# Kernel optimization log

Hardware: AMD Instinct MI355X
Metric: run time of the kernel (lower is better)

Reference implementation:

```python
import jax, jax.numpy as jnp
import numpy as np

NUM_HEADS = 8
NUM_POINTS = 4


def _bilinear(img, xs, ys):
    """Bilinear sample with zero padding (grid_sample align_corners=False).
    img: [N, H, W, C]; xs, ys: [N, P] pixel-space coords. Returns [N, P, C]."""
    H, W = img.shape[1], img.shape[2]
    x0 = jnp.floor(xs)
    y0 = jnp.floor(ys)
    wx = xs - x0
    wy = ys - y0
    x0i = x0.astype(jnp.int32)
    y0i = y0.astype(jnp.int32)

    def g(ix, iy):
        valid = ((ix >= 0) & (ix < W) & (iy >= 0) & (iy < H)).astype(img.dtype)
        ixc = jnp.clip(ix, 0, W - 1)
        iyc = jnp.clip(iy, 0, H - 1)
        v = jax.vmap(lambda im, yy, xx: im[yy, xx])(img, iyc, ixc)  # [N,P,C]
        return v * valid[..., None]

    return (g(x0i, y0i) * ((1 - wx) * (1 - wy))[..., None]
            + g(x0i + 1, y0i) * (wx * (1 - wy))[..., None]
            + g(x0i, y0i + 1) * ((1 - wx) * wy)[..., None]
            + g(x0i + 1, y0i + 1) * (wx * wy)[..., None])


def setup_inputs() -> dict:
    key = jax.random.key(0)
    ks = jax.random.split(key, 10)
    BN, C, H, W = 12, 256, 40, 100
    nq = H * W
    hp = NUM_HEADS * NUM_POINTS
    s = 1.0 / np.sqrt(C).astype(np.float32)
    return {
        "img_feats": jax.random.normal(ks[0], (BN, C, H, W), jnp.float32),
        "warp_grid": jax.random.uniform(ks[1], (BN, H, W, 2), jnp.float32),
        "reference_points": jax.random.uniform(ks[2], (BN, nq, 1, 2), jnp.float32),
        "Wv": jax.random.normal(ks[3], (C, C), jnp.float32) * s,
        "bv": jnp.zeros((C,), jnp.float32),
        "Woff": jax.random.normal(ks[4], (C, hp * 2), jnp.float32) * 0.01,
        "boff": jax.random.normal(ks[5], (hp * 2,), jnp.float32) * 0.5,
        "Wattn": jax.random.normal(ks[6], (C, hp), jnp.float32) * 0.01,
        "battn": jnp.zeros((hp,), jnp.float32),
        "Wout": jax.random.normal(ks[7], (C, C), jnp.float32) * s,
        "bout": jnp.zeros((C,), jnp.float32),
    }


def reference(img_feats, warp_grid, reference_points,
              Wv, bv, Woff, boff, Wattn, battn, Wout, bout):
    BN, C, H, W = img_feats.shape
    heads, pts = NUM_HEADS, NUM_POINTS
    hd = C // heads
    nq = H * W

    feat = img_feats.transpose(0, 2, 3, 1)  # [BN, H, W, C]

    # BEVWarp: bilinear warp of image features at the projected grid ([0,1] normed)
    gx = warp_grid[..., 0].reshape(BN, -1) * W - 0.5
    gy = warp_grid[..., 1].reshape(BN, -1) * H - 0.5
    warped = _bilinear(feat, gx, gy)          # [BN, nq, C] -> value
    query = feat.reshape(BN, nq, C)           # flattened img feats -> query

    # MultiScaleDeformableAttention, num_levels=1
    v = (warped @ Wv + bv).reshape(BN, nq, heads, hd)
    off = (query @ Woff + boff).reshape(BN, nq, heads, pts, 2)
    attn = jax.nn.softmax((query @ Wattn + battn).reshape(BN, nq, heads, pts), axis=-1)

    norm = jnp.array([W, H], dtype=img_feats.dtype)
    loc = reference_points.reshape(BN, nq, 1, 1, 2) + off / norm  # [BN,nq,h,p,2]

    vh = v.transpose(0, 2, 1, 3).reshape(BN * heads, H, W, hd)
    lx = (loc[..., 0] * W - 0.5).transpose(0, 2, 1, 3).reshape(BN * heads, nq * pts)
    ly = (loc[..., 1] * H - 0.5).transpose(0, 2, 1, 3).reshape(BN * heads, nq * pts)
    sampled = _bilinear(vh, lx, ly).reshape(BN, heads, nq, pts, hd)

    agg = jnp.einsum('bhqpd,bqhp->bqhd', sampled, attn).reshape(BN, nq, C)
    out = agg @ Wout + bout + query  # output_proj + residual (dropout=0 at eval)
    return out.transpose(0, 2, 1).reshape(BN, C, H, W)
```

## Files before the change

kernel.cpp:

```cpp
#include <hip/hip_runtime.h>

#define DEVINL __device__ __forceinline__

typedef __attribute__((ext_vector_type(4))) float f32x4;
typedef __attribute__((ext_vector_type(8))) short short8;

constexpr int kBN = 12, kC = 256, kH = 40, kW = 100;
constexpr int kNQ = kH * kW;
constexpr int kM = kBN * kNQ;

DEVINL float bflo(uint p) { union { uint i; float f; } v; v.i = p << 16; return v.f; }
DEVINL float bfhi(uint p) { union { uint i; float f; } v; v.i = p & 0xffff0000u; return v.f; }
DEVINL ushort f2bf(float f) {
  union { float f; uint i; } v; v.f = f;
  uint i = v.i;
  return (ushort)((i + 0x7fffu + ((i >> 16) & 1u)) >> 16);
}
DEVINL uint pack2(float a, float b) { return (uint)f2bf(a) | ((uint)f2bf(b) << 16); }

DEVINL void mfma_bf16(f32x4& acc, short8 a, short8 b) {
  acc = __builtin_amdgcn_mfma_f32_16x16x32_bf16(a, b, acc, 0, 0, 0);
}

DEVINL void gload16(const ushort* g, char* lds) {
  __builtin_amdgcn_global_load_lds(
      (const __attribute__((address_space(1))) uint*)g,
      (__attribute__((address_space(3))) uint*)lds, 16, 0, 0);
}

DEVINL void acc8(float* acc, uint4 d, float wv) {
  acc[0] += wv * bflo(d.x); acc[1] += wv * bfhi(d.x);
  acc[2] += wv * bflo(d.y); acc[3] += wv * bfhi(d.y);
  acc[4] += wv * bflo(d.z); acc[5] += wv * bfhi(d.z);
  acc[6] += wv * bflo(d.w); acc[7] += wv * bfhi(d.w);
}

__global__ __launch_bounds__(256) void k_wt_all(const float* __restrict__ Wv,
                                                const float* __restrict__ Woff,
                                                const float* __restrict__ Wattn,
                                                const float* __restrict__ Wout,
                                                ushort* __restrict__ WvT,
                                                ushort* __restrict__ WoffT,
                                                ushort* __restrict__ WattnT,
                                                ushort* __restrict__ WoutT) {
  int idx = blockIdx.x * 256 + threadIdx.x;
  const float* W; ushort* WT; int N, base;
  if (idx < 65536)       { W = Wv;    WT = WvT;    N = 256; base = 0; }
  else if (idx < 81920)  { W = Woff;  WT = WoffT;  N = 64;  base = 65536; }
  else if (idx < 90112)  { W = Wattn; WT = WattnT; N = 32;  base = 81920; }
  else if (idx < 155648) { W = Wout;  WT = WoutT;  N = 256; base = 90112; }
  else return;
  int i = idx - base;
  int n = i >> 8, k = i & 255;
  WT[i] = f2bf(W[k * N + n]);
}

__global__ __launch_bounds__(256) void k_transpose(const float* __restrict__ img,
                                                   ushort* __restrict__ feat) {
  __shared__ ushort tile[64][66];
  int b = blockIdx.z, c0 = blockIdx.y * 64, q0 = blockIdx.x * 64;
  int t = threadIdx.x;
  int ql = t & 63, cl = t >> 6;
#pragma unroll
  for (int i = 0; i < 16; ++i) {
    int c = cl + i * 4, q = q0 + ql;
    float v = (q < kNQ) ? img[(size_t)(b * kC + c0 + c) * kNQ + q] : 0.f;
    tile[c][ql] = f2bf(v);
  }
  __syncthreads();
#pragma unroll
  for (int i = 0; i < 2; ++i) {
    int idx = t + i * 256;
    int qlo = idx >> 3, cg = idx & 7;
    int q = q0 + qlo;
    if (q < kNQ) {
      ushort tmp[8];
#pragma unroll
      for (int j = 0; j < 8; ++j) tmp[j] = tile[cg * 8 + j][qlo];
      *(uint4*)(feat + ((size_t)b * kNQ + q) * kC + c0 + cg * 8) = *(uint4*)tmp;
    }
  }
}

__global__ __launch_bounds__(256) void k_warp(const ushort* __restrict__ feat,
                                              const float* __restrict__ grid,
                                              ushort* __restrict__ warped) {
  int orig = blockIdx.x;
  int n = (orig & 7) * 750 + (orig >> 3);
  int t = threadIdx.x;
  int ql = t >> 5, g = t & 31;
  int gq = n * 8 + ql;
  int b = gq / kNQ;
  float gx = grid[(size_t)gq * 2 + 0] * kW - 0.5f;
  float gy = grid[(size_t)gq * 2 + 1] * kH - 0.5f;
  float x0f = floorf(gx), y0f = floorf(gy);
  int x0 = (int)x0f, y0 = (int)y0f;
  float wx = gx - x0f, wy = gy - y0f;
  float acc[8];
#pragma unroll
  for (int i = 0; i < 8; ++i) acc[i] = 0.f;
  const ushort* fb = feat + (size_t)b * kNQ * kC + g * 8;
#pragma unroll
  for (int ty = 0; ty < 2; ++ty) {
    int iy = y0 + ty;
    if (iy < 0 || iy >= kH) continue;
    float wyv = ty ? wy : 1.f - wy;
#pragma unroll
    for (int tx = 0; tx < 2; ++tx) {
      int ix = x0 + tx;
      if (ix < 0 || ix >= kW) continue;
      float wv = wyv * (tx ? wx : 1.f - wx);
      uint4 d = *(const uint4*)(fb + (size_t)(iy * kW + ix) * kC);
      acc8(acc, d, wv);
    }
  }
  uint o[4] = {pack2(acc[0], acc[1]), pack2(acc[2], acc[3]),
               pack2(acc[4], acc[5]), pack2(acc[6], acc[7])};
  *(uint4*)(warped + (size_t)gq * kC + g * 8) = *(uint4*)o;
}

template <int EPI>
__global__ __launch_bounds__(256) void k_gemm256(const ushort* __restrict__ A,
                                                 const ushort* __restrict__ BT,
                                                 const float* __restrict__ bias,
                                                 ushort* __restrict__ Obf,
                                                 float* __restrict__ Ofp,
                                                 const float* __restrict__ resid) {
  extern __shared__ char smem[];
  const int t = threadIdx.x, wave = t >> 6, lane = t & 63;
  const int l15 = lane & 15, l4 = lane >> 4;
  const int b = blockIdx.x / 63, mb = blockIdx.x % 63;
  const int q0 = mb * 64;
  const int nrows = (kNQ - q0 < 64) ? (kNQ - q0) : 64;
  const int n0w = wave * 64;
  const int ra = t >> 2, ca = t & 3;
  const int rac = (ra < nrows) ? ra : (nrows - 1);
  const int sca = ca ^ ((ra >> 1) & 3);
  const ushort* gA = A + ((size_t)b * kNQ + q0 + rac) * 256 + sca * 8;
  const ushort* gB = BT + (size_t)ra * 256 + sca * 8;

  f32x4 acc[4][4];
#pragma unroll
  for (int i = 0; i < 4; ++i)
#pragma unroll
    for (int j = 0; j < 4; ++j) acc[i][j] = (f32x4)0.f;

  auto STAGE = [&](int buf, int kk) {
    char* Asb = smem + buf * 20480;
    char* Bsb = Asb + 4096;
    gload16(gA + kk, Asb + t * 16);
#pragma unroll
    for (int i = 0; i < 4; ++i)
      gload16(gB + (size_t)i * 64 * 256 + kk, Bsb + (i * 256 + t) * 16);
  };

  STAGE(0, 0);
  int cur = 0;
#pragma unroll 1
  for (int step = 0; step < 8; ++step) {
    if (step < 7) {
      STAGE(cur ^ 1, (step + 1) * 32);
      asm volatile("s_waitcnt vmcnt(5)" ::: "memory");
    } else {
      asm volatile("s_waitcnt vmcnt(0)" ::: "memory");
    }
    __builtin_amdgcn_s_barrier();
    asm volatile("" ::: "memory");
    char* Asb = smem + cur * 20480;
    char* Bsb = Asb + 4096;
    short8 af[4], bf[4];
#pragma unroll
    for (int mf = 0; mf < 4; ++mf) {
      int r = mf * 16 + l15;
      int sl = l4 ^ ((r >> 1) & 3);
      af[mf] = *(const short8*)(Asb + r * 64 + sl * 16);
    }
#pragma unroll
    for (int nf = 0; nf < 4; ++nf) {
      int r = n0w + nf * 16 + l15;
      int sl = l4 ^ ((r >> 1) & 3);
      bf[nf] = *(const short8*)(Bsb + r * 64 + sl * 16);
    }
#pragma unroll
    for (int mf = 0; mf < 4; ++mf)
#pragma unroll
      for (int nf = 0; nf < 4; ++nf) mfma_bf16(acc[mf][nf], af[mf], bf[nf]);
    asm volatile("" ::: "memory");
    __builtin_amdgcn_s_barrier();
    cur ^= 1;
  }

  if (EPI == 0) {
#pragma unroll
    for (int mf = 0; mf < 4; ++mf) {
      if (mf * 16 >= nrows) continue;
      int q = q0 + mf * 16 + l4 * 4;
#pragma unroll
      for (int nf = 0; nf < 4; ++nf) {
        int col = n0w + nf * 16 + l15;
        float bv = bias[col];
        int h = col >> 5, ch = col & 31;
        ushort* dst = Obf + (size_t)(b * 8 + h) * kNQ * 32 + ch;
#pragma unroll
        for (int j = 0; j < 4; ++j)
          dst[(size_t)(q + j) * 32] = f2bf(acc[mf][nf][j] + bv);
      }
    }
  } else {
    float* Tw = (float*)(smem + wave * 4352);
#pragma unroll
    for (int nf = 0; nf < 4; ++nf) {
      float bv = bias[n0w + nf * 16 + l15];
#pragma unroll
      for (int mf = 0; mf < 4; ++mf)
#pragma unroll
        for (int j = 0; j < 4; ++j)
          Tw[l15 * 68 + mf * 16 + l4 * 4 + j] = acc[mf][nf][j] + bv;
      int c = l15, rs = l4 * 16;
      if (rs < nrows) {
        int col = n0w + nf * 16 + c;
        size_t gi = ((size_t)b * kC + col) * kNQ + q0 + rs;
#pragma unroll
        for (int k = 0; k < 4; ++k) {
          float4 tv = *(float4*)(&Tw[c * 68 + rs + k * 4]);
          float4 rv = *(const float4*)(resid + gi + k * 4);
          tv.x += rv.x; tv.y += rv.y; tv.z += rv.z; tv.w += rv.w;
          *(float4*)(Ofp + gi + k * 4) = tv;
        }
      }
    }
  }
}

__global__ __launch_bounds__(256) void k_offattn(const ushort* __restrict__ A,
                                                 const ushort* __restrict__ WoffT,
                                                 const ushort* __restrict__ WattnT,
                                                 const float* __restrict__ boff,
                                                 const float* __restrict__ battn,
                                                 const float* __restrict__ refp,
                                                 float* __restrict__ samp) {
  extern __shared__ char smem[];
  float* T = (float*)smem;
  const int t = threadIdx.x, wave = t >> 6, lane = t & 63;
  const int l15 = lane & 15, l4 = lane >> 4;
  const int b = blockIdx.x / 63, mb = blockIdx.x % 63;
  const int q0 = mb * 64;
  const int nrows = (kNQ - q0 < 64) ? (kNQ - q0) : 64;
  const int wr = wave >> 1, wc = wave & 1;
  const int ra = t >> 2, ca = t & 3;
  const int rac = (ra < nrows) ? ra : (nrows - 1);
  const int sca = ca ^ ((ra >> 1) & 3);
  const ushort* gA  = A + ((size_t)b * kNQ + q0 + rac) * 256 + sca * 8;
  const ushort* gB0 = WoffT + (size_t)ra * 256 + sca * 8;
  const ushort* gB1 = WattnT + (size_t)ra * 256 + sca * 8;

  f32x4 acc[2][3];
#pragma unroll
  for (int i = 0; i < 2; ++i)
#pragma unroll
    for (int j = 0; j < 3; ++j) acc[i][j] = (f32x4)0.f;

  auto STAGE = [&](int buf, int kk) {
    char* Asb = smem + buf * 10240;
    char* Bsb = Asb + 4096;
    gload16(gA + kk, Asb + t * 16);
    gload16(gB0 + kk, Bsb + t * 16);
    if (t < 128) gload16(gB1 + kk, Bsb + (256 + t) * 16);
  };

  STAGE(0, 0);
  int cur = 0;
#pragma unroll 1
  for (int step = 0; step < 8; ++step) {
    if (step < 7) {
      STAGE(cur ^ 1, (step + 1) * 32);
      if (wave < 2) asm volatile("s_waitcnt vmcnt(3)" ::: "memory");
      else          asm volatile("s_waitcnt vmcnt(2)" ::: "memory");
    } else {
      asm volatile("s_waitcnt vmcnt(0)" ::: "memory");
    }
    __builtin_amdgcn_s_barrier();
    asm volatile("" ::: "memory");
    char* Asb = smem + cur * 10240;
    char* Bsb = Asb + 4096;
    short8 af[2], bf[3];
#pragma unroll
    for (int mf = 0; mf < 2; ++mf) {
      int r = wr * 32 + mf * 16 + l15;
      int sl = l4 ^ ((r >> 1) & 3);
      af[mf] = *(const short8*)(Asb + r * 64 + sl * 16);
    }
#pragma unroll
    for (int nf = 0; nf < 3; ++nf) {
      int r = wc * 48 + nf * 16 + l15;
      int sl = l4 ^ ((r >> 1) & 3);
      bf[nf] = *(const short8*)(Bsb + r * 64 + sl * 16);
    }
#pragma unroll
    for (int mf = 0; mf < 2; ++mf)
#pragma unroll
      for (int nf = 0; nf < 3; ++nf) mfma_bf16(acc[mf][nf], af[mf], bf[nf]);
    asm volatile("" ::: "memory");
    __builtin_amdgcn_s_barrier();
    cur ^= 1;
  }

#pragma unroll
  for (int nf = 0; nf < 3; ++nf) {
    int col = wc * 48 + nf * 16 + l15;
    float bv = (col < 64) ? boff[col] : battn[col - 64];
#pragma unroll
    for (int mf = 0; mf < 2; ++mf)
#pragma unroll
      for (int j = 0; j < 4; ++j) {
        int row = wr * 32 + mf * 16 + l4 * 4 + j;
        T[row * 101 + col] = acc[mf][nf][j] + bv;
      }
  }
  __syncthreads();
  int row = t >> 2;
  if (row < nrows) {
    int q = q0 + row;
    float refx = refp[((size_t)b * kNQ + q) * 2 + 0] * kW - 0.5f;
    float refy = refp[((size_t)b * kNQ + q) * 2 + 1] * kH - 0.5f;
#pragma unroll
    for (int hi2 = 0; hi2 < 2; ++hi2) {
      int h = (t & 3) + hi2 * 4;
      float sx[4], sy[4], lg[4];
#pragma unroll
      for (int p = 0; p < 4; ++p) {
        sx[p] = refx + T[row * 101 + h * 8 + p * 2 + 0];
        sy[p] = refy + T[row * 101 + h * 8 + p * 2 + 1];
        lg[p] = T[row * 101 + 64 + h * 4 + p];
      }
      float mx = fmaxf(fmaxf(lg[0], lg[1]), fmaxf(lg[2], lg[3]));
      float e[4], s = 0.f;
#pragma unroll
      for (int p = 0; p < 4; ++p) { e[p] = __expf(lg[p] - mx); s += e[p]; }
      float inv = 1.f / s;
      float* dst = samp + (((size_t)(b * 8 + h) * kNQ + q) * 4) * 3;
#pragma unroll
      for (int p = 0; p < 4; ++p) {
        dst[p * 3 + 0] = sx[p];
        dst[p * 3 + 1] = sy[p];
        dst[p * 3 + 2] = e[p] * inv;
      }
    }
  }
}

__global__ __launch_bounds__(256) void k_sample(const ushort* __restrict__ v,
                                                const float* __restrict__ samp,
                                                ushort* __restrict__ agg) {
  int orig = blockIdx.x;
  int n = (orig & 7) * 756 + (orig >> 3);
  int plane = n / 63, chunk = n - plane * 63;
  int t = threadIdx.x;
  int ql = t >> 2, g = t & 3;
  int q = chunk * 64 + ql;
  if (q >= kNQ) return;
  int b = plane >> 3, h = plane & 7;
  const ushort* pv = v + (size_t)plane * kNQ * 32 + g * 8;
  const int lane = t & 63, gbase = lane & ~3;

  const float* sp = samp + (((size_t)plane * kNQ + q) * 4 + g) * 3;
  float myx = sp[0], myy = sp[1], myw = sp[2];
  float acc[8];
#pragma unroll
  for (int i = 0; i < 8; ++i) acc[i] = 0.f;
#pragma unroll
  for (int p = 0; p < 4; ++p) {
    float sxp = __shfl(myx, gbase + p);
    float syp = __shfl(myy, gbase + p);
    float wp  = __shfl(myw, gbase + p);
    float x0f = floorf(sxp), y0f = floorf(syp);
    int x0 = (int)x0f, y0 = (int)y0f;
    float wx = sxp - x0f, wy = syp - y0f;
#pragma unroll
    for (int ty = 0; ty < 2; ++ty) {
      int iy = y0 + ty;
      if (iy < 0 || iy >= kH) continue;
      float wyv = ty ? wy : 1.f - wy;
#pragma unroll
      for (int tx = 0; tx < 2; ++tx) {
        int ix = x0 + tx;
        if (ix < 0 || ix >= kW) continue;
        float wv = wp * wyv * (tx ? wx : 1.f - wx);
        uint4 d = *(const uint4*)(pv + (size_t)(iy * kW + ix) * 32);
        acc8(acc, d, wv);
      }
    }
  }
  uint o[4] = {pack2(acc[0], acc[1]), pack2(acc[2], acc[3]),
               pack2(acc[4], acc[5]), pack2(acc[6], acc[7])};
  *(uint4*)(agg + ((size_t)b * kNQ + q) * kC + h * 32 + g * 8) = *(uint4*)o;
}

extern "C" void kernel_launch(void* const* d_in, const int* in_sizes, int n_in,
                              void* d_out, int out_size, void* d_ws, size_t ws_size,
                              hipStream_t stream) {
  const float* img   = (const float*)d_in[0];
  const float* grid  = (const float*)d_in[1];
  const float* refp  = (const float*)d_in[2];
  const float* Wv    = (const float*)d_in[3];
  const float* bv    = (const float*)d_in[4];
  const float* Woff  = (const float*)d_in[5];
  const float* boff  = (const float*)d_in[6];
  const float* Wattn = (const float*)d_in[7];
  const float* battn = (const float*)d_in[8];
  const float* Wout  = (const float*)d_in[9];
  const float* bout  = (const float*)d_in[10];
  float* out = (float*)d_out;

  char* ws = (char*)d_ws;
  const size_t SZ = (size_t)kM * kC * 2;
  ushort* feat   = (ushort*)(ws);
  ushort* warped = (ushort*)(ws + SZ);
  ushort* vbuf   = (ushort*)(ws + 2 * SZ);
  float*  samp   = (float*)(ws + 3 * SZ);
  ushort* WvT    = (ushort*)(ws + 4 * SZ);
  ushort* WoffT  = (ushort*)(ws + 4 * SZ + 131072);
  ushort* WattnT = (ushort*)(ws + 4 * SZ + 131072 + 32768);
  ushort* WoutT  = (ushort*)(ws + 4 * SZ + 131072 + 32768 + 16384);
  ushort* aggb   = warped;

  k_wt_all<<<608, 256, 0, stream>>>(Wv, Woff, Wattn, Wout, WvT, WoffT, WattnT, WoutT);
  k_transpose<<<dim3(63, 4, 12), 256, 0, stream>>>(img, feat);
  k_warp<<<6000, 256, 0, stream>>>(feat, grid, warped);
  k_gemm256<0><<<756, 256, 40960, stream>>>(warped, WvT, bv, vbuf, nullptr, nullptr);
  k_offattn<<<756, 256, 25856, stream>>>(feat, WoffT, WattnT, boff, battn, refp, samp);
  k_sample<<<6048, 256, 0, stream>>>(vbuf, samp, aggb);
  k_gemm256<1><<<756, 256, 40960, stream>>>(aggb, WoutT, bout, nullptr, out, img);
}
```

Baseline: 122.6 us.

## Merge prep, warp and offset/attention kernels; read residual from bf16 features

Combines the input transpose with weight conversion into one launch, and the bilinear warp with the offset/attention GEMM into one launch via block-index dispatch. This cuts the launch count and lets independent stages overlap. The output GEMM now reads the residual from the bf16 transposed feature buffer instead of fp32 input. That lowers precision and uses strided 2-byte loads. Warp blocks now also reserve shared memory they do not use, which may reduce occupancy.

Result: faster. 115.0 us (-6.2%).

```diff
diff --git a/kernel.cpp b/kernel.cpp
--- a/kernel.cpp
+++ b/kernel.cpp
@@ -35,97 +35,216 @@
   acc[6] += wv * bflo(d.w); acc[7] += wv * bfhi(d.w);
 }
 
-__global__ __launch_bounds__(256) void k_wt_all(const float* __restrict__ Wv,
-                                                const float* __restrict__ Woff,
-                                                const float* __restrict__ Wattn,
-                                                const float* __restrict__ Wout,
-                                                ushort* __restrict__ WvT,
-                                                ushort* __restrict__ WoffT,
-                                                ushort* __restrict__ WattnT,
-                                                ushort* __restrict__ WoutT) {
-  int idx = blockIdx.x * 256 + threadIdx.x;
-  const float* W; ushort* WT; int N, base;
-  if (idx < 65536)       { W = Wv;    WT = WvT;    N = 256; base = 0; }
-  else if (idx < 81920)  { W = Woff;  WT = WoffT;  N = 64;  base = 65536; }
-  else if (idx < 90112)  { W = Wattn; WT = WattnT; N = 32;  base = 81920; }
-  else if (idx < 155648) { W = Wout;  WT = WoutT;  N = 256; base = 90112; }
-  else return;
-  int i = idx - base;
-  int n = i >> 8, k = i & 255;
-  WT[i] = f2bf(W[k * N + n]);
-}
-
-__global__ __launch_bounds__(256) void k_transpose(const float* __restrict__ img,
-                                                   ushort* __restrict__ feat) {
+__global__ __launch_bounds__(256) void k_prep(const float* __restrict__ img,
+                                              ushort* __restrict__ feat,
+                                              const float* __restrict__ Wv,
+                                              const float* __restrict__ Woff,
+                                              const float* __restrict__ Wattn,
+                                              const float* __restrict__ Wout,
+                                              ushort* __restrict__ WvT,
+                                              ushort* __restrict__ WoffT,
+                                              ushort* __restrict__ WattnT,
+                                              ushort* __restrict__ WoutT) {
   __shared__ ushort tile[64][66];
-  int b = blockIdx.z, c0 = blockIdx.y * 64, q0 = blockIdx.x * 64;
-  int t = threadIdx.x;
-  int ql = t & 63, cl = t >> 6;
-#pragma unroll
-  for (int i = 0; i < 16; ++i) {
-    int c = cl + i * 4, q = q0 + ql;
-    float v = (q < kNQ) ? img[(size_t)(b * kC + c0 + c) * kNQ + q] : 0.f;
-    tile[c][ql] = f2bf(v);
+  int bx = blockIdx.x, t = threadIdx.x;
+  if (bx < 3024) {
+    int qb = bx % 63, cb = (bx / 63) & 3, b = bx / 252;
+    int c0 = cb * 64, q0 = qb * 64;
+    int ql = t & 63, cl = t >> 6;
+#pragma unroll
+    for (int i = 0; i < 16; ++i) {
+      int c = cl + i * 4, q = q0 + ql;
+      float v = (q < kNQ) ? img[(size_t)(b * kC + c0 + c) * kNQ + q] : 0.f;
+      tile[c][ql] = f2bf(v);
+    }
+    __syncthreads();
+#pragma unroll
+    for (int i = 0; i < 2; ++i) {
+      int idx = t + i * 256;
+      int qlo = idx >> 3, cg = idx & 7;
+      int q = q0 + qlo;
+      if (q < kNQ) {
+        ushort tmp[8];
+#pragma unroll
+        for (int j = 0; j < 8; ++j) tmp[j] = tile[cg * 8 + j][qlo];
+        *(uint4*)(feat + ((size_t)b * kNQ + q) * kC + c0 + cg * 8) = *(uint4*)tmp;
+      }
+    }
+  } else {
+    int idx = (bx - 3024) * 256 + t;
+    const float* W; ushort* WT; int N, base;
+    if (idx < 65536)       { W = Wv;    WT = WvT;    N = 256; base = 0; }
+    else if (idx < 81920)  { W = Woff;  WT = WoffT;  N = 64;  base = 65536; }
+    else if (idx < 90112)  { W = Wattn; WT = WattnT; N = 32;  base = 81920; }
+    else if (idx < 155648) { W = Wout;  WT = WoutT;  N = 256; base = 90112; }
+    else return;
+    int i = idx - base;
+    int n = i >> 8, k = i & 255;
+    WT[i] = f2bf(W[k * N + n]);
+  }
+}
+
+__global__ __launch_bounds__(256) void k_warp_offattn(const ushort* __restrict__ feat,
+                                                      const float* __restrict__ grid,
+                                                      ushort* __restrict__ warped,
+                                                      const ushort* __restrict__ WoffT,
+                                                      const ushort* __restrict__ WattnT,
+                                                      const float* __restrict__ boff,
+                                                      const float* __restrict__ battn,
+                                                      const float* __restrict__ refp,
+                                                      float* __restrict__ samp) {
+  extern __shared__ char smem[];
+  const int t = threadIdx.x;
+  int bx = blockIdx.x;
+
+  if (bx >= 756) {
+    int orig = bx - 756;
+    int n = (orig & 7) * 750 + (orig >> 3);
+    int ql = t >> 5, g = t & 31;
+    int gq = n * 8 + ql;
+    int b = gq / kNQ;
+    float gx = grid[(size_t)gq * 2 + 0] * kW - 0.5f;
+    float gy = grid[(size_t)gq * 2 + 1] * kH - 0.5f;
+    float x0f = floorf(gx), y0f = floorf(gy);
+    int x0 = (int)x0f, y0 = (int)y0f;
+    float wx = gx - x0f, wy = gy - y0f;
+    float acc[8];
+#pragma unroll
+    for (int i = 0; i < 8; ++i) acc[i] = 0.f;
+    const ushort* fb = feat + (size_t)b * kNQ * kC + g * 8;
+#pragma unroll
+    for (int ty = 0; ty < 2; ++ty) {
+      int iy = y0 + ty;
+      if (iy < 0 || iy >= kH) continue;
+      float wyv = ty ? wy : 1.f - wy;
+#pragma unroll
+      for (int tx = 0; tx < 2; ++tx) {
+        int ix = x0 + tx;
+        if (ix < 0 || ix >= kW) continue;
+        float wv = wyv * (tx ? wx : 1.f - wx);
+        uint4 d = *(const uint4*)(fb + (size_t)(iy * kW + ix) * kC);
+        acc8(acc, d, wv);
+      }
+    }
+    uint o[4] = {pack2(acc[0], acc[1]), pack2(acc[2], acc[3]),
+                 pack2(acc[4], acc[5]), pack2(acc[6], acc[7])};
+    *(uint4*)(warped + (size_t)gq * kC + g * 8) = *(uint4*)o;
+    return;
+  }
+
+  float* T = (float*)smem;
+  const int wave = t >> 6, lane = t & 63;
+  const int l15 = lane & 15, l4 = lane >> 4;
+  const int b = bx / 63, mb = bx % 63;
+  const int q0 = mb * 64;
+  const int nrows = (kNQ - q0 < 64) ? (kNQ - q0) : 64;
+  const int wr = wave >> 1, wc = wave & 1;
+  const int ra = t >> 2, ca = t & 3;
+  const int rac = (ra < nrows) ? ra : (nrows - 1);
+  const int sca = ca ^ ((ra >> 1) & 3);
+  const ushort* gA  = feat + ((size_t)b * kNQ + q0 + rac) * 256 + sca * 8;
+  const ushort* gB0 = WoffT + (size_t)ra * 256 + sca * 8;
+  const ushort* gB1 = WattnT + (size_t)ra * 256 + sca * 8;
+
+  f32x4 acc[2][3];
+#pragma unroll
+  for (int i = 0; i < 2; ++i)
+#pragma unroll
+    for (int j = 0; j < 3; ++j) acc[i][j] = (f32x4)0.f;
+
+  auto STAGE = [&](int buf, int kk) {
+    char* Asb = smem + buf * 10240;
+    char* Bsb = Asb + 4096;
+    gload16(gA + kk, Asb + t * 16);
+    gload16(gB0 + kk, Bsb + t * 16);
+    if (t < 128) gload16(gB1 + kk, Bsb + (256 + t) * 16);
+  };
+
+  STAGE(0, 0);
+  int cur = 0;
+#pragma unroll 1
+  for (int step = 0; step < 8; ++step) {
+    if (step < 7) {
+      STAGE(cur ^ 1, (step + 1) * 32);
+      if (wave < 2) asm volatile("s_waitcnt vmcnt(3)" ::: "memory");
+      else          asm volatile("s_waitcnt vmcnt(2)" ::: "memory");
+    } else {
+      asm volatile("s_waitcnt vmcnt(0)" ::: "memory");
+    }
+    __builtin_amdgcn_s_barrier();
+    asm volatile("" ::: "memory");
+    char* Asb = smem + cur * 10240;
+    char* Bsb = Asb + 4096;
+    short8 af[2], bf[3];
+#pragma unroll
+    for (int mf = 0; mf < 2; ++mf) {
+      int r = wr * 32 + mf * 16 + l15;
+      int sl = l4 ^ ((r >> 1) & 3);
+      af[mf] = *(const short8*)(Asb + r * 64 + sl * 16);
+    }
+#pragma unroll
+    for (int nf = 0; nf < 3; ++nf) {
+      int r = wc * 48 + nf * 16 + l15;
+      int sl = l4 ^ ((r >> 1) & 3);
+      bf[nf] = *(const short8*)(Bsb + r * 64 + sl * 16);
+    }
+#pragma unroll
+    for (int mf = 0; mf < 2; ++mf)
+#pragma unroll
+      for (int nf = 0; nf < 3; ++nf) mfma_bf16(acc[mf][nf], af[mf], bf[nf]);
+    asm volatile("" ::: "memory");
+    __builtin_amdgcn_s_barrier();
+    cur ^= 1;
+  }
+
+#pragma unroll
+  for (int nf = 0; nf < 3; ++nf) {
+    int col = wc * 48 + nf * 16 + l15;
+    float bv = (col < 64) ? boff[col] : battn[col - 64];
+#pragma unroll
+    for (int mf = 0; mf < 2; ++mf)
+#pragma unroll
+      for (int j = 0; j < 4; ++j) {
+        int row = wr * 32 + mf * 16 + l4 * 4 + j;
+        T[row * 101 + col] = acc[mf][nf][j] + bv;
+      }
   }
   __syncthreads();
-#pragma unroll
-  for (int i = 0; i < 2; ++i) {
-    int idx = t + i * 256;
-    int qlo = idx >> 3, cg = idx & 7;
-    int q = q0 + qlo;
-    if (q < kNQ) {
-      ushort tmp[8];
-#pragma unroll
-      for (int j = 0; j < 8; ++j) tmp[j] = tile[cg * 8 + j][qlo];
-      *(uint4*)(feat + ((size_t)b * kNQ + q) * kC + c0 + cg * 8) = *(uint4*)tmp;
-    }
-  }
-}
-
-__global__ __launch_bounds__(256) void k_warp(const ushort* __restrict__ feat,
-                                              const float* __restrict__ grid,
-                                              ushort* __restrict__ warped) {
-  int orig = blockIdx.x;
-  int n = (orig & 7) * 750 + (orig >> 3);
-  int t = threadIdx.x;
-  int ql = t >> 5, g = t & 31;
-  int gq = n * 8 + ql;
-  int b = gq / kNQ;
-  float gx = grid[(size_t)gq * 2 + 0] * kW - 0.5f;
-  float gy = grid[(size_t)gq * 2 + 1] * kH - 0.5f;
-  float x0f = floorf(gx), y0f = floorf(gy);
-  int x0 = (int)x0f, y0 = (int)y0f;
-  float wx = gx - x0f, wy = gy - y0f;
-  float acc[8];
-#pragma unroll
-  for (int i = 0; i < 8; ++i) acc[i] = 0.f;
-  const ushort* fb = feat + (size_t)b * kNQ * kC + g * 8;
-#pragma unroll
-  for (int ty = 0; ty < 2; ++ty) {
-    int iy = y0 + ty;
-    if (iy < 0 || iy >= kH) continue;
-    float wyv = ty ? wy : 1.f - wy;
-#pragma unroll
-    for (int tx = 0; tx < 2; ++tx) {
-      int ix = x0 + tx;
-      if (ix < 0 || ix >= kW) continue;
-      float wv = wyv * (tx ? wx : 1.f - wx);
-      uint4 d = *(const uint4*)(fb + (size_t)(iy * kW + ix) * kC);
-      acc8(acc, d, wv);
-    }
-  }
-  uint o[4] = {pack2(acc[0], acc[1]), pack2(acc[2], acc[3]),
-               pack2(acc[4], acc[5]), pack2(acc[6], acc[7])};
-  *(uint4*)(warped + (size_t)gq * kC + g * 8) = *(uint4*)o;
-}
-
-template <int EPI>
-__global__ __launch_bounds__(256) void k_gemm256(const ushort* __restrict__ A,
-                                                 const ushort* __restrict__ BT,
-                                                 const float* __restrict__ bias,
-                                                 ushort* __restrict__ Obf,
-                                                 float* __restrict__ Ofp,
-                                                 const float* __restrict__ resid) {
+  int row = t >> 2;
+  if (row < nrows) {
+    int q = q0 + row;
+    float refx = refp[((size_t)b * kNQ + q) * 2 + 0] * kW - 0.5f;
+    float refy = refp[((size_t)b * kNQ + q) * 2 + 1] * kH - 0.5f;
+#pragma unroll
+    for (int hi2 = 0; hi2 < 2; ++hi2) {
+      int h = (t & 3) + hi2 * 4;
+      float sx[4], sy[4], lg[4];
+#pragma unroll
+      for (int p = 0; p < 4; ++p) {
+        sx[p] = refx + T[row * 101 + h * 8 + p * 2 + 0];
+        sy[p] = refy + T[row * 101 + h * 8 + p * 2 + 1];
+        lg[p] = T[row * 101 + 64 + h * 4 + p];
+      }
+      float mx = fmaxf(fmaxf(lg[0], lg[1]), fmaxf(lg[2], lg[3]));
+      float e[4], s = 0.f;
+#pragma unroll
+      for (int p = 0; p < 4; ++p) { e[p] = __expf(lg[p] - mx); s += e[p]; }
+      float inv = 1.f / s;
+      float* dst = samp + (((size_t)(b * 8 + h) * kNQ + q) * 4) * 3;
+#pragma unroll
+      for (int p = 0; p < 4; ++p) {
+        dst[p * 3 + 0] = sx[p];
+        dst[p * 3 + 1] = sy[p];
+        dst[p * 3 + 2] = e[p] * inv;
+      }
+    }
+  }
+}
+
+__global__ __launch_bounds__(256) void k_gemmv(const ushort* __restrict__ A,
+                                               const ushort* __restrict__ BT,
+                                               const float* __restrict__ bias,
+                                               ushort* __restrict__ Obf) {
   extern __shared__ char smem[];
   const int t = threadIdx.x, wave = t >> 6, lane = t & 63;
   const int l15 = lane & 15, l4 = lane >> 4;
@@ -190,161 +309,19 @@
     cur ^= 1;
   }
 
-  if (EPI == 0) {
-#pragma unroll
-    for (int mf = 0; mf < 4; ++mf) {
-      if (mf * 16 >= nrows) continue;
-      int q = q0 + mf * 16 + l4 * 4;
-#pragma unroll
-      for (int nf = 0; nf < 4; ++nf) {
-        int col = n0w + nf * 16 + l15;
-        float bv = bias[col];
-        int h = col >> 5, ch = col & 31;
-        ushort* dst = Obf + (size_t)(b * 8 + h) * kNQ * 32 + ch;
-#pragma unroll
-        for (int j = 0; j < 4; ++j)
-          dst[(size_t)(q + j) * 32] = f2bf(acc[mf][nf][j] + bv);
-      }
-    }
-  } else {
-    float* Tw = (float*)(smem + wave * 4352);
+#pragma unroll
+  for (int mf = 0; mf < 4; ++mf) {
+    if (mf * 16 >= nrows) continue;
+    int q = q0 + mf * 16 + l4 * 4;
 #pragma unroll
     for (int nf = 0; nf < 4; ++nf) {
-      float bv = bias[n0w + nf * 16 + l15];
-#pragma unroll
-      for (int mf = 0; mf < 4; ++mf)
-#pragma unroll
-        for (int j = 0; j < 4; ++j)
-          Tw[l15 * 68 + mf * 16 + l4 * 4 + j] = acc[mf][nf][j] + bv;
-      int c = l15, rs = l4 * 16;
-      if (rs < nrows) {
-        int col = n0w + nf * 16 + c;
-        size_t gi = ((size_t)b * kC + col) * kNQ + q0 + rs;
-#pragma unroll
-        for (int k = 0; k < 4; ++k) {
-          float4 tv = *(float4*)(&Tw[c * 68 + rs + k * 4]);
-          float4 rv = *(const float4*)(resid + gi + k * 4);
-          tv.x += rv.x; tv.y += rv.y; tv.z += rv.z; tv.w += rv.w;
-          *(float4*)(Ofp + gi + k * 4) = tv;
-        }
-      }
-    }
-  }
-}
-
-__global__ __launch_bounds__(256) void k_offattn(const ushort* __restrict__ A,
-                                                 const ushort* __restrict__ WoffT,
-                                                 const ushort* __restrict__ WattnT,
-                                                 const float* __restrict__ boff,
-                                                 const float* __restrict__ battn,
-                                                 const float* __restrict__ refp,
-                                                 float* __restrict__ samp) {
-  extern __shared__ char smem[];
-  float* T = (float*)smem;
-  const int t = threadIdx.x, wave = t >> 6, lane = t & 63;
-  const int l15 = lane & 15, l4 = lane >> 4;
-  const int b = blockIdx.x / 63, mb = blockIdx.x % 63;
-  const int q0 = mb * 64;
-  const int nrows = (kNQ - q0 < 64) ? (kNQ - q0) : 64;
-  const int wr = wave >> 1, wc = wave & 1;
-  const int ra = t >> 2, ca = t & 3;
-  const int rac = (ra < nrows) ? ra : (nrows - 1);
-  const int sca = ca ^ ((ra >> 1) & 3);
-  const ushort* gA  = A + ((size_t)b * kNQ + q0 + rac) * 256 + sca * 8;
-  const ushort* gB0 = WoffT + (size_t)ra * 256 + sca * 8;
-  const ushort* gB1 = WattnT + (size_t)ra * 256 + sca * 8;
-
-  f32x4 acc[2][3];
-#pragma unroll
-  for (int i = 0; i < 2; ++i)
-#pragma unroll
-    for (int j = 0; j < 3; ++j) acc[i][j] = (f32x4)0.f;
-
-  auto STAGE = [&](int buf, int kk) {
-    char* Asb = smem + buf * 10240;
-    char* Bsb = Asb + 4096;
-    gload16(gA + kk, Asb + t * 16);
-    gload16(gB0 + kk, Bsb + t * 16);
-    if (t < 128) gload16(gB1 + kk, Bsb + (256 + t) * 16);
-  };
-
-  STAGE(0, 0);
-  int cur = 0;
-#pragma unroll 1
-  for (int step = 0; step < 8; ++step) {
-    if (step < 7) {
-      STAGE(cur ^ 1, (step + 1) * 32);
-      if (wave < 2) asm volatile("s_waitcnt vmcnt(3)" ::: "memory");
-      else          asm volatile("s_waitcnt vmcnt(2)" ::: "memory");
-    } else {
-      asm volatile("s_waitcnt vmcnt(0)" ::: "memory");
-    }
-    __builtin_amdgcn_s_barrier();
-    asm volatile("" ::: "memory");
-    char* Asb = smem + cur * 10240;
-    char* Bsb = Asb + 4096;
-    short8 af[2], bf[3];
-#pragma unroll
-    for (int mf = 0; mf < 2; ++mf) {
-      int r = wr * 32 + mf * 16 + l15;
-      int sl = l4 ^ ((r >> 1) & 3);
-      af[mf] = *(const short8*)(Asb + r * 64 + sl * 16);
-    }
-#pragma unroll
-    for (int nf = 0; nf < 3; ++nf) {
-      int r = wc * 48 + nf * 16 + l15;
-      int sl = l4 ^ ((r >> 1) & 3);
-      bf[nf] = *(const short8*)(Bsb + r * 64 + sl * 16);
-    }
-#pragma unroll
-    for (int mf = 0; mf < 2; ++mf)
-#pragma unroll
-      for (int nf = 0; nf < 3; ++nf) mfma_bf16(acc[mf][nf], af[mf], bf[nf]);
-    asm volatile("" ::: "memory");
-    __builtin_amdgcn_s_barrier();
-    cur ^= 1;
-  }
-
-#pragma unroll
-  for (int nf = 0; nf < 3; ++nf) {
-    int col = wc * 48 + nf * 16 + l15;
-    float bv = (col < 64) ? boff[col] : battn[col - 64];
-#pragma unroll
-    for (int mf = 0; mf < 2; ++mf)
-#pragma unroll
-      for (int j = 0; j < 4; ++j) {
-        int row = wr * 32 + mf * 16 + l4 * 4 + j;
-        T[row * 101 + col] = acc[mf][nf][j] + bv;
-      }
-  }
-  __syncthreads();
-  int row = t >> 2;
-  if (row < nrows) {
-    int q = q0 + row;
-    float refx = refp[((size_t)b * kNQ + q) * 2 + 0] * kW - 0.5f;
-    float refy = refp[((size_t)b * kNQ + q) * 2 + 1] * kH - 0.5f;
-#pragma unroll
-    for (int hi2 = 0; hi2 < 2; ++hi2) {
-      int h = (t & 3) + hi2 * 4;
-      float sx[4], sy[4], lg[4];
-#pragma unroll
-      for (int p = 0; p < 4; ++p) {
-        sx[p] = refx + T[row * 101 + h * 8 + p * 2 + 0];
-        sy[p] = refy + T[row * 101 + h * 8 + p * 2 + 1];
-        lg[p] = T[row * 101 + 64 + h * 4 + p];
-      }
-      float mx = fmaxf(fmaxf(lg[0], lg[1]), fmaxf(lg[2], lg[3]));
-      float e[4], s = 0.f;
-#pragma unroll
-      for (int p = 0; p < 4; ++p) { e[p] = __expf(lg[p] - mx); s += e[p]; }
-      float inv = 1.f / s;
-      float* dst = samp + (((size_t)(b * 8 + h) * kNQ + q) * 4) * 3;
-#pragma unroll
-      for (int p = 0; p < 4; ++p) {
-        dst[p * 3 + 0] = sx[p];
-        dst[p * 3 + 1] = sy[p];
-        dst[p * 3 + 2] = e[p] * inv;
-      }
+      int col = n0w + nf * 16 + l15;
+      float bv = bias[col];
+      int h = col >> 5, ch = col & 31;
+      ushort* dst = Obf + (size_t)(b * 8 + h) * kNQ * 32 + ch;
+#pragma unroll
+      for (int j = 0; j < 4; ++j)
+        dst[(size_t)(q + j) * 32] = f2bf(acc[mf][nf][j] + bv);
     }
   }
 }
@@ -394,6 +371,102 @@
   uint o[4] = {pack2(acc[0], acc[1]), pack2(acc[2], acc[3]),
                pack2(acc[4], acc[5]), pack2(acc[6], acc[7])};
   *(uint4*)(agg + ((size_t)b * kNQ + q) * kC + h * 32 + g * 8) = *(uint4*)o;
+}
+
+__global__ __launch_bounds__(256) void k_gemmout(const ushort* __restrict__ A,
+                                                 const ushort* __restrict__ BT,
+                                                 const float* __restrict__ bias,
+                                                 float* __restrict__ Ofp,
+                                                 const ushort* __restrict__ feat) {
+  extern __shared__ char smem[];
+  const int t = threadIdx.x, wave = t >> 6, lane = t & 63;
+  const int l15 = lane & 15, l4 = lane >> 4;
+  const int b = blockIdx.x / 63, mb = blockIdx.x % 63;
+  const int q0 = mb * 64;
+  const int nrows = (kNQ - q0 < 64) ? (kNQ - q0) : 64;
+  const int n0w = wave * 64;
+  const int ra = t >> 2, ca = t & 3;
+  const int rac = (ra < nrows) ? ra : (nrows - 1);
+  const int sca = ca ^ ((ra >> 1) & 3);
+  const ushort* gA = A + ((size_t)b * kNQ + q0 + rac) * 256 + sca * 8;
+  const ushort* gB = BT + (size_t)ra * 256 + sca * 8;
+
+  f32x4 acc[4][4];
+#pragma unroll
+  for (int i = 0; i < 4; ++i)
+#pragma unroll
+    for (int j = 0; j < 4; ++j) acc[i][j] = (f32x4)0.f;
+
+  auto STAGE = [&](int buf, int kk) {
+    char* Asb = smem + buf * 20480;
+    char* Bsb = Asb + 4096;
+    gload16(gA + kk, Asb + t * 16);
+#pragma unroll
+    for (int i = 0; i < 4; ++i)
+      gload16(gB + (size_t)i * 64 * 256 + kk, Bsb + (i * 256 + t) * 16);
+  };
+
+  STAGE(0, 0);
+  int cur = 0;
+#pragma unroll 1
+  for (int step = 0; step < 8; ++step) {
+    if (step < 7) {
+      STAGE(cur ^ 1, (step + 1) * 32);
+      asm volatile("s_waitcnt vmcnt(5)" ::: "memory");
+    } else {
+      asm volatile("s_waitcnt vmcnt(0)" ::: "memory");
+    }
+    __builtin_amdgcn_s_barrier();
+    asm volatile("" ::: "memory");
+    char* Asb = smem + cur * 20480;
+    char* Bsb = Asb + 4096;
+    short8 af[4], bf[4];
+#pragma unroll
+    for (int mf = 0; mf < 4; ++mf) {
+      int r = mf * 16 + l15;
+      int sl = l4 ^ ((r >> 1) & 3);
+      af[mf] = *(const short8*)(Asb + r * 64 + sl * 16);
+    }
+#pragma unroll
+    for (int nf = 0; nf < 4; ++nf) {
+      int r = n0w + nf * 16 + l15;
+      int sl = l4 ^ ((r >> 1) & 3);
+      bf[nf] = *(const short8*)(Bsb + r * 64 + sl * 16);
+    }
+#pragma unroll
+    for (int mf = 0; mf < 4; ++mf)
+#pragma unroll
+      for (int nf = 0; nf < 4; ++nf) mfma_bf16(acc[mf][nf], af[mf], bf[nf]);
+    asm volatile("" ::: "memory");
+    __builtin_amdgcn_s_barrier();
+    cur ^= 1;
+  }
+
+  float* Tw = (float*)(smem + wave * 4352);
+#pragma unroll
+  for (int nf = 0; nf < 4; ++nf) {
+    float bv = bias[n0w + nf * 16 + l15];
+#pragma unroll
+    for (int mf = 0; mf < 4; ++mf)
+#pragma unroll
+      for (int j = 0; j < 4; ++j)
+        Tw[l15 * 68 + mf * 16 + l4 * 4 + j] = acc[mf][nf][j] + bv;
+    int c = l15, rs = l4 * 16;
+    if (rs < nrows) {
+      int col = n0w + nf * 16 + c;
+      size_t gi = ((size_t)b * kC + col) * kNQ + q0 + rs;
+      const ushort* fr = feat + ((size_t)b * kNQ + q0 + rs) * kC + col;
+#pragma unroll
+      for (int k = 0; k < 4; ++k) {
+        float4 tv = *(float4*)(&Tw[c * 68 + rs + k * 4]);
+        tv.x += bflo(fr[(size_t)(k * 4 + 0) * kC]);
+        tv.y += bflo(fr[(size_t)(k * 4 + 1) * kC]);
+        tv.z += bflo(fr[(size_t)(k * 4 + 2) * kC]);
+        tv.w += bflo(fr[(size_t)(k * 4 + 3) * kC]);
+        *(float4*)(Ofp + gi + k * 4) = tv;
+      }
+    }
+  }
 }
 
 extern "C" void kernel_launch(void* const* d_in, const int* in_sizes, int n_in,
@@ -424,11 +497,11 @@
   ushort* WoutT  = (ushort*)(ws + 4 * SZ + 131072 + 32768 + 16384);
   ushort* aggb   = warped;
 
-  k_wt_all<<<608, 256, 0, stream>>>(Wv, Woff, Wattn, Wout, WvT, WoffT, WattnT, WoutT);
-  k_transpose<<<dim3(63, 4, 12), 256, 0, stream>>>(img, feat);
-  k_warp<<<6000, 256, 0, stream>>>(feat, grid, warped);
-  k_gemm256<0><<<756, 256, 40960, stream>>>(warped, WvT, bv, vbuf, nullptr, nullptr);
-  k_offattn<<<756, 256, 25856, stream>>>(feat, WoffT, WattnT, boff, battn, refp, samp);
+  k_prep<<<3632, 256, 0, stream>>>(img, feat, Wv, Woff, Wattn, Wout,
+                                   WvT, WoffT, WattnT, WoutT);
+  k_warp_offattn<<<6756, 256, 25856, stream>>>(feat, grid, warped, WoffT, WattnT,
+                                               boff, battn, refp, samp);
+  k_gemmv<<<756, 256, 40960, stream>>>(warped, WvT, bv, vbuf);
   k_sample<<<6048, 256, 0, stream>>>(vbuf, samp, aggb);
-  k_gemm256<1><<<756, 256, 40960, stream>>>(aggb, WoutT, bout, nullptr, out, img);
-}
+  k_gemmout<<<756, 256, 40960, stream>>>(aggb, WoutT, bout, out, feat);
+}
```
